# Kernel optimization log

Hardware: AMD Instinct MI355X
Metric: run time of the kernel (lower is better)

The kernel has to match this reference:

```python
import jax, jax.numpy as jnp
import numpy as np

B, S, V, E, U, L = 32, 256, 32000, 512, 512, 2

def setup_inputs() -> dict:
    key = jax.random.key(0)
    ks = jax.random.split(key, 16)
    def p(k, shape, scale):
        return jax.random.normal(k, shape, dtype=jnp.float32) * scale
    inp = {
        "x": jax.random.randint(ks[0], (B, S), 0, V),
        "state": jnp.zeros((2 * L, B, U), jnp.float32),
        "emb_table": p(ks[1], (V, E), 0.05),
    }
    names = ["fk0", "frk0", "fb0", "fk1", "frk1", "fb1",
             "bk0", "brk0", "bb0", "bk1", "brk1", "bb1"]
    i = 2
    for n in names:
        if n.endswith("b0") or n.endswith("b1"):
            inp[n] = jnp.zeros((2, 3 * U), jnp.float32)
        else:
            inp[n] = p(ks[i], (512, 3 * U), 1.0 / np.sqrt(512))
        i += 1
    return inp

def gru_step(h, xt, k, rk, b):
    # TF2 GRUCell, reset_after=True
    mx = xt @ k + b[0]
    mi = h @ rk + b[1]
    xz, xr, xh = jnp.split(mx, 3, axis=-1)
    iz, ir, ih = jnp.split(mi, 3, axis=-1)
    z = jax.nn.sigmoid(xz + iz)
    r = jax.nn.sigmoid(xr + ir)
    hh = jnp.tanh(xh + r * ih)
    return z * h + (1.0 - z) * hh

def run_rnn(emb_s, mask_s, h0s, params):
    # emb_s: [S,B,E], mask_s: [S,B], h0s: tuple of L x [B,U]
    def step(carry, inp):
        hs, prev = carry
        xt, mt = inp
        m = mt[:, None]
        new_hs = []
        a = xt
        for h, (k, rk, b) in zip(hs, params):
            hn = gru_step(h, a, k, rk, b)
            hn = jnp.where(m, hn, h)  # masked steps carry state
            new_hs.append(hn)
            a = hn
        out = jnp.where(m, a, prev)  # masked steps repeat prev output
        return (tuple(new_hs), out), out
    init = (tuple(h0s), jnp.zeros((emb_s.shape[1], U), emb_s.dtype))
    (hs_f, _), ys = jax.lax.scan(step, init, (emb_s, mask_s))
    return ys, hs_f

def reference(x, state, emb_table,
              fk0, frk0, fb0, fk1, frk1, fb1,
              bk0, brk0, bb0, bk1, brk1, bb1):
    emb = emb_table[x]                      # [B,S,E]
    mask = (x != 0)                         # mask_zero=True
    emb_s = jnp.swapaxes(emb, 0, 1)         # [S,B,E]
    mask_s = jnp.swapaxes(mask, 0, 1)       # [S,B]
    fw_params = [(fk0, frk0, fb0), (fk1, frk1, fb1)]
    bw_params = [(bk0, brk0, bb0), (bk1, brk1, bb1)]
    ys_f, hs_f = run_rnn(emb_s, mask_s, (state[0], state[1]), fw_params)
    ys_b, hs_b = run_rnn(emb_s[::-1], mask_s[::-1], (state[2], state[3]), bw_params)
    ys_b = ys_b[::-1]
    y = jnp.concatenate([ys_f, ys_b], axis=-1)   # [S,B,2U]
    y = jnp.swapaxes(y, 0, 1)                    # [B,S,2U]
    states = jnp.stack(list(hs_f) + list(hs_b), axis=0)  # [2L,B,U]
    return y, states
```

## Files before the change

### kernel.cpp

```cpp
#include <hip/hip_runtime.h>
#include <hip/hip_bf16.h>

#define S_LEN 256
#define NB 32
#define UDIM 512
#define WGS 32
#define NH 16

typedef __attribute__((ext_vector_type(8))) short bf16x8;
typedef __attribute__((ext_vector_type(4))) float f32x4;
typedef __attribute__((ext_vector_type(4))) unsigned u32x4;

struct WPtrs { const float* p[8]; };
struct BPtrs { const float* p[4]; };

__device__ __forceinline__ unsigned short f2bf(float f) {
  union { float f; unsigned u; } v; v.f = f;
  unsigned r = v.u + 0x7fffu + ((v.u >> 16) & 1u);
  return (unsigned short)(r >> 16);
}

__device__ __forceinline__ int ld_flag(const int* p) {
  int v;
  asm volatile("global_load_dword %0, %1, off sc0 sc1\n\ts_waitcnt vmcnt(0)"
               : "=&v"(v) : "v"(p) : "memory");
  return v;
}
__device__ __forceinline__ void st_u32c(unsigned* p, unsigned v) {
  asm volatile("global_store_dword %0, %1, off sc0 sc1" :: "v"(p), "v"(v) : "memory");
}
__device__ __forceinline__ void st_flag(int* p, int v) {
  asm volatile("global_store_dword %0, %1, off sc0 sc1" :: "v"(p), "v"(v) : "memory");
}
__device__ __forceinline__ void ld_hist16(const short* p0, const short* p1,
                                          bf16x8* afr0, bf16x8* afr1) {
  u32x4 q0,q1,q2,q3,q4,q5,q6,q7,q8,q9,q10,q11,q12,q13,q14,q15;
  asm volatile(
    "global_load_dwordx4 %0, %16, off sc0 sc1\n\t"
    "global_load_dwordx4 %1, %16, off offset:64 sc0 sc1\n\t"
    "global_load_dwordx4 %2, %16, off offset:128 sc0 sc1\n\t"
    "global_load_dwordx4 %3, %16, off offset:192 sc0 sc1\n\t"
    "global_load_dwordx4 %4, %16, off offset:256 sc0 sc1\n\t"
    "global_load_dwordx4 %5, %16, off offset:320 sc0 sc1\n\t"
    "global_load_dwordx4 %6, %16, off offset:384 sc0 sc1\n\t"
    "global_load_dwordx4 %7, %16, off offset:448 sc0 sc1\n\t"
    "global_load_dwordx4 %8, %17, off sc0 sc1\n\t"
    "global_load_dwordx4 %9, %17, off offset:64 sc0 sc1\n\t"
    "global_load_dwordx4 %10, %17, off offset:128 sc0 sc1\n\t"
    "global_load_dwordx4 %11, %17, off offset:192 sc0 sc1\n\t"
    "global_load_dwordx4 %12, %17, off offset:256 sc0 sc1\n\t"
    "global_load_dwordx4 %13, %17, off offset:320 sc0 sc1\n\t"
    "global_load_dwordx4 %14, %17, off offset:384 sc0 sc1\n\t"
    "global_load_dwordx4 %15, %17, off offset:448 sc0 sc1\n\t"
    "s_waitcnt vmcnt(0)"
    : "=&v"(q0),"=&v"(q1),"=&v"(q2),"=&v"(q3),"=&v"(q4),"=&v"(q5),"=&v"(q6),"=&v"(q7),
      "=&v"(q8),"=&v"(q9),"=&v"(q10),"=&v"(q11),"=&v"(q12),"=&v"(q13),"=&v"(q14),"=&v"(q15)
    : "v"(p0), "v"(p1)
    : "memory");
  union U { u32x4 u; bf16x8 b; } cv;
  cv.u=q0;  afr0[0]=cv.b; cv.u=q1;  afr0[1]=cv.b; cv.u=q2;  afr0[2]=cv.b; cv.u=q3;  afr0[3]=cv.b;
  cv.u=q4;  afr0[4]=cv.b; cv.u=q5;  afr0[5]=cv.b; cv.u=q6;  afr0[6]=cv.b; cv.u=q7;  afr0[7]=cv.b;
  cv.u=q8;  afr1[0]=cv.b; cv.u=q9;  afr1[1]=cv.b; cv.u=q10; afr1[2]=cv.b; cv.u=q11; afr1[3]=cv.b;
  cv.u=q12; afr1[4]=cv.b; cv.u=q13; afr1[5]=cv.b; cv.u=q14; afr1[6]=cv.b; cv.u=q15; afr1[7]=cv.b;
}

__global__ void k_embed(const int* __restrict__ x, const float* __restrict__ tab,
                        unsigned short* __restrict__ emb, int* __restrict__ mask) {
  int t = blockIdx.x, b = blockIdx.y;
  int tok = x[b * S_LEN + t];
  if (threadIdx.x == 0) mask[t * NB + b] = (tok != 0);
  const float4* src = (const float4*)(tab + (size_t)tok * UDIM);
  ushort4* dst = (ushort4*)(emb + ((size_t)t * NB + b) * UDIM);
  int i = threadIdx.x;
  float4 v = src[i];
  ushort4 o;
  o.x = f2bf(v.x); o.y = f2bf(v.y); o.z = f2bf(v.z); o.w = f2bf(v.w);
  dst[i] = o;
}

__global__ void k_wprep(WPtrs wp, unsigned short* __restrict__ wsW) {
  int bid = blockIdx.x;
  int kt = bid & 31; bid >>= 5;
  int g  = bid % 3;  bid /= 3;
  int wg = bid & 31; bid >>= 5;
  int slab = bid;
  const float* src = wp.p[slab];
  int tid = threadIdx.x;
  int r = tid >> 4, cc = tid & 15;
  __shared__ float ldsT[16][17];
  ldsT[cc][r] = src[(size_t)(kt * 16 + r) * 1536 + g * 512 + wg * 16 + cc];
  __syncthreads();
  size_t off = ((size_t)slab * WGS + wg) * (48 * 512) + (size_t)(g * 16 + r) * 512 + kt * 16 + cc;
  wsW[off] = f2bf(ldsT[r][cc]);
}

__global__ __launch_bounds__(256, 1) void k_rnn(
    const unsigned short* __restrict__ wsW, const unsigned short* __restrict__ emb,
    unsigned short* __restrict__ hist, const int* __restrict__ mask,
    int* __restrict__ flags, const float* __restrict__ state,
    BPtrs bp, float* __restrict__ out) {
  __shared__ short sW[2 * 48 * 512];
  __shared__ float sAcc[2][2][32][48];
  __shared__ float sBias[2][48];
  __shared__ unsigned char sMask[S_LEN][NB];

  int tid = threadIdx.x;
  int bid = blockIdx.x;
  int xcd = bid & 7;
  int c = xcd >> 1;
  int w = ((bid >> 3) << 1) | (xcd & 1);
  int layer = c & 1;
  bool back = (c >= 2);
  int lane = tid & 63;
  int wave = tid >> 6;
  int mat = wave & 1;
  int kh = wave >> 1;

  int cb = tid >> 3;
  int cj = (tid & 7) << 1;
  float hreg0, hreg1, preg0 = 0.f, preg1 = 0.f;

  {
    const size_t slabSz = 48 * 512;
    for (int ch = tid; ch < 2 * 48 * 64; ch += 256) {
      int m = ch / (48 * 64);
      int rem = ch % (48 * 64);
      int nl = rem >> 6;
      int k16 = rem & 63;
      const unsigned short* sp =
          wsW + ((size_t)((c * 2 + m) * WGS) + w) * slabSz + (size_t)nl * 512 + k16 * 8;
      bf16x8 val = *(const bf16x8*)sp;
      int byte = m * 49152 + nl * 1024 + ((k16 * 16) ^ ((nl & 7) << 4));
      *(bf16x8*)((char*)sW + byte) = val;
    }
    const float* bptr = bp.p[c];
    for (int i = tid; i < 96; i += 256) {
      int m = i / 48, nl = i % 48;
      int col = (nl / 16) * 512 + w * 16 + (nl & 15);
      sBias[m][nl] = bptr[m * 1536 + col];
    }
    for (int i = tid; i < S_LEN * NB; i += 256)
      sMask[i >> 5][i & 31] = (unsigned char)(mask[i] != 0);
    int col = w * 16 + cj;
    hreg0 = state[((size_t)c * NB + cb) * UDIM + col];
    hreg1 = state[((size_t)c * NB + cb) * UDIM + col + 1];
    unsigned pk = (unsigned)f2bf(hreg0) | ((unsigned)f2bf(hreg1) << 16);
    st_u32c((unsigned*)(hist + (((size_t)c * 257) * NB + cb) * UDIM + col), pk);
  }
  asm volatile("s_waitcnt vmcnt(0)" ::: "memory");
  __syncthreads();
  if (tid == 0) st_flag(&flags[(c * 257) * 32 + w], 1);

  for (int t = 0; t < S_LEN; ++t) {
    int treal = back ? (S_LEN - 1 - t) : t;
    const unsigned short* arow;
    const int* fl = nullptr;
    int ownIdx = -1;
    if (mat == 0) {
      if (layer == 0) {
        arow = emb + (size_t)treal * NB * UDIM;
      } else {
        arow = hist + ((size_t)(c - 1) * 257 + (t + 1)) * NB * UDIM;
        fl = flags + ((c - 1) * 257 + (t + 1)) * 32;
      }
    } else {
      arow = hist + ((size_t)c * 257 + t) * NB * UDIM;
      fl = flags + (c * 257 + t) * 32;
      ownIdx = w;
    }

    int r15 = lane & 15, quad = lane >> 4;
    const short* a16 = (const short*)arow;
    int abase = r15 * UDIM + kh * 256 + quad * 8;

    bf16x8 afr0[8], afr1[8];
    if (fl) {
      const int* fp = fl + (lane & 31);
      bool sub = ((lane & 31) == ownIdx);
      int v = sub ? 1 : ld_flag(fp);
      while (!__all(v != 0)) {
        __builtin_amdgcn_s_sleep(1);
        v = sub ? 1 : ld_flag(fp);
      }
      ld_hist16((const short*)(a16 + abase), (const short*)(a16 + abase + 16 * UDIM),
                afr0, afr1);
    } else {
#pragma unroll
      for (int kc = 0; kc < 8; ++kc) {
        afr0[kc] = *(const bf16x8*)(a16 + abase + kc * 32);
        afr1[kc] = *(const bf16x8*)(a16 + abase + 16 * UDIM + kc * 32);
      }
    }

    f32x4 acc[2][3];
#pragma unroll
    for (int a = 0; a < 2; a++)
#pragma unroll
      for (int g = 0; g < 3; g++) acc[a][g] = (f32x4){0.f, 0.f, 0.f, 0.f};
    int matbase = mat * 49152;
#pragma unroll
    for (int kc = 0; kc < 8; ++kc) {
#pragma unroll
      for (int g = 0; g < 3; ++g) {
        int nl = g * 16 + r15;
        int koff = kh * 512 + kc * 64 + quad * 16;
        int byte = matbase + nl * 1024 + (koff ^ ((nl & 7) << 4));
        bf16x8 bw = *(const bf16x8*)((const char*)sW + byte);
        acc[0][g] = __builtin_amdgcn_mfma_f32_16x16x32_bf16(afr0[kc], bw, acc[0][g], 0, 0, 0);
        acc[1][g] = __builtin_amdgcn_mfma_f32_16x16x32_bf16(afr1[kc], bw, acc[1][g], 0, 0, 0);
      }
    }
#pragma unroll
    for (int mt = 0; mt < 2; ++mt)
#pragma unroll
      for (int g = 0; g < 3; ++g)
#pragma unroll
        for (int rr = 0; rr < 4; ++rr)
          sAcc[kh][mat][mt * 16 + quad * 4 + rr][g * 16 + r15] = acc[mt][g][rr];
    __syncthreads();

    {
      int b = cb, j0 = cj;
      bool m = sMask[treal][b] != 0;
      float hn0, hn1;
#pragma unroll
      for (int u = 0; u < 2; ++u) {
        int j = j0 + u;
        float az = sAcc[0][0][b][j]      + sAcc[1][0][b][j]      + sBias[0][j];
        float ar = sAcc[0][0][b][16 + j] + sAcc[1][0][b][16 + j] + sBias[0][16 + j];
        float ah = sAcc[0][0][b][32 + j] + sAcc[1][0][b][32 + j] + sBias[0][32 + j];
        float iz = sAcc[0][1][b][j]      + sAcc[1][1][b][j]      + sBias[1][j];
        float ir = sAcc[0][1][b][16 + j] + sAcc[1][1][b][16 + j] + sBias[1][16 + j];
        float ih = sAcc[0][1][b][32 + j] + sAcc[1][1][b][32 + j] + sBias[1][32 + j];
        float z = 1.f / (1.f + __expf(-(az + iz)));
        float r = 1.f / (1.f + __expf(-(ar + ir)));
        float pre = ah + r * ih;
        pre = fminf(fmaxf(pre, -30.f), 30.f);
        float e2 = __expf(2.f * pre);
        float hh = (e2 - 1.f) / (e2 + 1.f);
        float hold = (u == 0) ? hreg0 : hreg1;
        float hv = z * hold + (1.f - z) * hh;
        hv = m ? hv : hold;
        if (u == 0) hn0 = hv; else hn1 = hv;
      }
      hreg0 = hn0; hreg1 = hn1;
      unsigned pk = (unsigned)f2bf(hn0) | ((unsigned)f2bf(hn1) << 16);
      st_u32c((unsigned*)(hist + (((size_t)c * 257 + (t + 1)) * NB + b) * UDIM + w * 16 + j0), pk);
      if (layer == 1) {
        float o0 = m ? hn0 : preg0;
        float o1 = m ? hn1 : preg1;
        preg0 = o0; preg1 = o1;
        *(float2*)(out + ((size_t)b * S_LEN + treal) * 1024 + (back ? 512 : 0) + w * 16 + j0) =
            make_float2(o0, o1);
      }
      if (t == S_LEN - 1) {
        *(float2*)(out + (size_t)NB * S_LEN * 1024 + ((size_t)c * NB + b) * UDIM + w * 16 + j0) =
            make_float2(hn0, hn1);
      }
    }
    asm volatile("s_waitcnt vmcnt(0)" ::: "memory");
    __syncthreads();
    if (tid == 0) st_flag(&flags[(c * 257 + (t + 1)) * 32 + w], 1);
  }
}

extern "C" void kernel_launch(void* const* d_in, const int* in_sizes, int n_in,
                              void* d_out, int out_size, void* d_ws, size_t ws_size,
                              hipStream_t stream) {
  const int* x = (const int*)d_in[0];
  const float* state = (const float*)d_in[1];
  const float* tab = (const float*)d_in[2];
  WPtrs wp;
  wp.p[0] = (const float*)d_in[3];
  wp.p[1] = (const float*)d_in[4];
  wp.p[2] = (const float*)d_in[6];
  wp.p[3] = (const float*)d_in[7];
  wp.p[4] = (const float*)d_in[9];
  wp.p[5] = (const float*)d_in[10];
  wp.p[6] = (const float*)d_in[12];
  wp.p[7] = (const float*)d_in[13];
  BPtrs bp;
  bp.p[0] = (const float*)d_in[5];
  bp.p[1] = (const float*)d_in[8];
  bp.p[2] = (const float*)d_in[11];
  bp.p[3] = (const float*)d_in[14];
  float* out = (float*)d_out;

  char* ws = (char*)d_ws;
  size_t off = 0;
  unsigned short* wsW = (unsigned short*)(ws + off); off += (size_t)8 * 32 * 48 * 512 * 2;
  unsigned short* embp = (unsigned short*)(ws + off); off += (size_t)S_LEN * NB * UDIM * 2;
  unsigned short* hist = (unsigned short*)(ws + off); off += (size_t)4 * 257 * NB * UDIM * 2;
  int* maskp = (int*)(ws + off); off += (size_t)S_LEN * NB * 4;
  int* flags = (int*)(ws + off); off += (size_t)4 * 257 * 32 * 4;

  hipMemsetAsync(flags, 0, (size_t)4 * 257 * 32 * 4, stream);
  k_embed<<<dim3(S_LEN, NB), 128, 0, stream>>>(x, tab, embp, maskp);
  k_wprep<<<8 * 32 * 3 * 32, 256, 0, stream>>>(wp, wsW);
  k_rnn<<<128, 256, 0, stream>>>(wsW, embp, hist, maskp, flags, state, bp, out);
}
```

Baseline: 1.137 ms.

## Replace per-step flag handshakes with sentinel-filled history polling

Drops the separate flag array and its per-step store/poll handshake. The history buffer is now pre-filled with 0xFF and consumers spin directly on the history data until no sentinel words remain. The sAcc buffer is double-buffered by step parity so the trailing barrier and vmcnt wait at the end of each step can be removed. This cuts one round trip and one barrier per step, but adds a large memset of the history buffer. Correctness now depends on computed bf16 pairs never equalling 0xFFFFFFFF, which is a NaN pattern, and on each 32-bit word being stored atomically.

```diff
diff --git a/kernel.cpp b/kernel.cpp
--- a/kernel.cpp
+++ b/kernel.cpp
@@ -20,19 +20,11 @@
   return (unsigned short)(r >> 16);
 }
 
-__device__ __forceinline__ int ld_flag(const int* p) {
-  int v;
-  asm volatile("global_load_dword %0, %1, off sc0 sc1\n\ts_waitcnt vmcnt(0)"
-               : "=&v"(v) : "v"(p) : "memory");
-  return v;
-}
 __device__ __forceinline__ void st_u32c(unsigned* p, unsigned v) {
   asm volatile("global_store_dword %0, %1, off sc0 sc1" :: "v"(p), "v"(v) : "memory");
 }
-__device__ __forceinline__ void st_flag(int* p, int v) {
-  asm volatile("global_store_dword %0, %1, off sc0 sc1" :: "v"(p), "v"(v) : "memory");
-}
-__device__ __forceinline__ void ld_hist16(const short* p0, const short* p1,
+
+__device__ __forceinline__ bool ld_hist16(const short* p0, const short* p1,
                                           bf16x8* afr0, bf16x8* afr1) {
   u32x4 q0,q1,q2,q3,q4,q5,q6,q7,q8,q9,q10,q11,q12,q13,q14,q15;
   asm volatile(
@@ -57,11 +49,18 @@
       "=&v"(q8),"=&v"(q9),"=&v"(q10),"=&v"(q11),"=&v"(q12),"=&v"(q13),"=&v"(q14),"=&v"(q15)
     : "v"(p0), "v"(p1)
     : "memory");
+  const unsigned S = 0xFFFFFFFFu;
+  bool bad = false;
+#define CK(q) bad |= (q[0]==S)|(q[1]==S)|(q[2]==S)|(q[3]==S)
+  CK(q0);CK(q1);CK(q2);CK(q3);CK(q4);CK(q5);CK(q6);CK(q7);
+  CK(q8);CK(q9);CK(q10);CK(q11);CK(q12);CK(q13);CK(q14);CK(q15);
+#undef CK
   union U { u32x4 u; bf16x8 b; } cv;
   cv.u=q0;  afr0[0]=cv.b; cv.u=q1;  afr0[1]=cv.b; cv.u=q2;  afr0[2]=cv.b; cv.u=q3;  afr0[3]=cv.b;
   cv.u=q4;  afr0[4]=cv.b; cv.u=q5;  afr0[5]=cv.b; cv.u=q6;  afr0[6]=cv.b; cv.u=q7;  afr0[7]=cv.b;
   cv.u=q8;  afr1[0]=cv.b; cv.u=q9;  afr1[1]=cv.b; cv.u=q10; afr1[2]=cv.b; cv.u=q11; afr1[3]=cv.b;
   cv.u=q12; afr1[4]=cv.b; cv.u=q13; afr1[5]=cv.b; cv.u=q14; afr1[6]=cv.b; cv.u=q15; afr1[7]=cv.b;
+  return !bad;
 }
 
 __global__ void k_embed(const int* __restrict__ x, const float* __restrict__ tab,
@@ -97,10 +96,9 @@
 __global__ __launch_bounds__(256, 1) void k_rnn(
     const unsigned short* __restrict__ wsW, const unsigned short* __restrict__ emb,
     unsigned short* __restrict__ hist, const int* __restrict__ mask,
-    int* __restrict__ flags, const float* __restrict__ state,
-    BPtrs bp, float* __restrict__ out) {
+    const float* __restrict__ state, BPtrs bp, float* __restrict__ out) {
   __shared__ short sW[2 * 48 * 512];
-  __shared__ float sAcc[2][2][32][48];
+  __shared__ float sAcc[2][2][2][32][48];
   __shared__ float sBias[2][48];
   __shared__ unsigned char sMask[S_LEN][NB];
 
@@ -147,26 +145,18 @@
     unsigned pk = (unsigned)f2bf(hreg0) | ((unsigned)f2bf(hreg1) << 16);
     st_u32c((unsigned*)(hist + (((size_t)c * 257) * NB + cb) * UDIM + col), pk);
   }
-  asm volatile("s_waitcnt vmcnt(0)" ::: "memory");
   __syncthreads();
-  if (tid == 0) st_flag(&flags[(c * 257) * 32 + w], 1);
 
   for (int t = 0; t < S_LEN; ++t) {
+    int p = t & 1;
     int treal = back ? (S_LEN - 1 - t) : t;
     const unsigned short* arow;
-    const int* fl = nullptr;
-    int ownIdx = -1;
+    bool coh;
     if (mat == 0) {
-      if (layer == 0) {
-        arow = emb + (size_t)treal * NB * UDIM;
-      } else {
-        arow = hist + ((size_t)(c - 1) * 257 + (t + 1)) * NB * UDIM;
-        fl = flags + ((c - 1) * 257 + (t + 1)) * 32;
-      }
+      if (layer == 0) { arow = emb + (size_t)treal * NB * UDIM; coh = false; }
+      else { arow = hist + ((size_t)(c - 1) * 257 + (t + 1)) * NB * UDIM; coh = true; }
     } else {
-      arow = hist + ((size_t)c * 257 + t) * NB * UDIM;
-      fl = flags + (c * 257 + t) * 32;
-      ownIdx = w;
+      arow = hist + ((size_t)c * 257 + t) * NB * UDIM; coh = true;
     }
 
     int r15 = lane & 15, quad = lane >> 4;
@@ -174,16 +164,12 @@
     int abase = r15 * UDIM + kh * 256 + quad * 8;
 
     bf16x8 afr0[8], afr1[8];
-    if (fl) {
-      const int* fp = fl + (lane & 31);
-      bool sub = ((lane & 31) == ownIdx);
-      int v = sub ? 1 : ld_flag(fp);
-      while (!__all(v != 0)) {
+    if (coh) {
+      bool ok = ld_hist16(a16 + abase, a16 + abase + 16 * UDIM, afr0, afr1);
+      while (!__all(ok)) {
         __builtin_amdgcn_s_sleep(1);
-        v = sub ? 1 : ld_flag(fp);
-      }
-      ld_hist16((const short*)(a16 + abase), (const short*)(a16 + abase + 16 * UDIM),
-                afr0, afr1);
+        ok = ld_hist16(a16 + abase, a16 + abase + 16 * UDIM, afr0, afr1);
+      }
     } else {
 #pragma unroll
       for (int kc = 0; kc < 8; ++kc) {
@@ -216,7 +202,7 @@
       for (int g = 0; g < 3; ++g)
 #pragma unroll
         for (int rr = 0; rr < 4; ++rr)
-          sAcc[kh][mat][mt * 16 + quad * 4 + rr][g * 16 + r15] = acc[mt][g][rr];
+          sAcc[p][kh][mat][mt * 16 + quad * 4 + rr][g * 16 + r15] = acc[mt][g][rr];
     __syncthreads();
 
     {
@@ -226,12 +212,12 @@
 #pragma unroll
       for (int u = 0; u < 2; ++u) {
         int j = j0 + u;
-        float az = sAcc[0][0][b][j]      + sAcc[1][0][b][j]      + sBias[0][j];
-        float ar = sAcc[0][0][b][16 + j] + sAcc[1][0][b][16 + j] + sBias[0][16 + j];
-        float ah = sAcc[0][0][b][32 + j] + sAcc[1][0][b][32 + j] + sBias[0][32 + j];
-        float iz = sAcc[0][1][b][j]      + sAcc[1][1][b][j]      + sBias[1][j];
-        float ir = sAcc[0][1][b][16 + j] + sAcc[1][1][b][16 + j] + sBias[1][16 + j];
-        float ih = sAcc[0][1][b][32 + j] + sAcc[1][1][b][32 + j] + sBias[1][32 + j];
+        float az = sAcc[p][0][0][b][j]      + sAcc[p][1][0][b][j]      + sBias[0][j];
+        float ar = sAcc[p][0][0][b][16 + j] + sAcc[p][1][0][b][16 + j] + sBias[0][16 + j];
+        float ah = sAcc[p][0][0][b][32 + j] + sAcc[p][1][0][b][32 + j] + sBias[0][32 + j];
+        float iz = sAcc[p][0][1][b][j]      + sAcc[p][1][1][b][j]      + sBias[1][j];
+        float ir = sAcc[p][0][1][b][16 + j] + sAcc[p][1][1][b][16 + j] + sBias[1][16 + j];
+        float ih = sAcc[p][0][1][b][32 + j] + sAcc[p][1][1][b][32 + j] + sBias[1][32 + j];
         float z = 1.f / (1.f + __expf(-(az + iz)));
         float r = 1.f / (1.f + __expf(-(ar + ir)));
         float pre = ah + r * ih;
@@ -258,9 +244,6 @@
             make_float2(hn0, hn1);
       }
     }
-    asm volatile("s_waitcnt vmcnt(0)" ::: "memory");
-    __syncthreads();
-    if (tid == 0) st_flag(&flags[(c * 257 + (t + 1)) * 32 + w], 1);
   }
 }
 
@@ -290,12 +273,12 @@
   size_t off = 0;
   unsigned short* wsW = (unsigned short*)(ws + off); off += (size_t)8 * 32 * 48 * 512 * 2;
   unsigned short* embp = (unsigned short*)(ws + off); off += (size_t)S_LEN * NB * UDIM * 2;
-  unsigned short* hist = (unsigned short*)(ws + off); off += (size_t)4 * 257 * NB * UDIM * 2;
+  unsigned short* hist = (unsigned short*)(ws + off);
+  size_t histBytes = (size_t)4 * 257 * NB * UDIM * 2;  off += histBytes;
   int* maskp = (int*)(ws + off); off += (size_t)S_LEN * NB * 4;
-  int* flags = (int*)(ws + off); off += (size_t)4 * 257 * 32 * 4;
-
-  hipMemsetAsync(flags, 0, (size_t)4 * 257 * 32 * 4, stream);
+
+  hipMemsetAsync(hist, 0xFF, histBytes, stream);
   k_embed<<<dim3(S_LEN, NB), 128, 0, stream>>>(x, tab, embp, maskp);
   k_wprep<<<8 * 32 * 3 * 32, 256, 0, stream>>>(wp, wsW);
-  k_rnn<<<128, 256, 0, stream>>>(wsW, embp, hist, maskp, flags, state, bp, out);
-}
+  k_rnn<<<128, 256, 0, stream>>>(wsW, embp, hist, maskp, state, bp, out);
+}
```

Result: slower. 1.475 ms (+29.8%).
